# Optimization experiments

Measured on AMD Instinct MI355X. Metric: run time of the kernel, lower is better.

The kernel has to match this reference:

```python
import jax, jax.numpy as jnp
import numpy as np

N_VAR, N_CHK, DV, DC = 8192, 4096, 3, 6
N_EDGE = N_VAR * DV  # == N_CHK * DC = 24576
BATCH = 512
N_ITER = 5
EPS = 1e-12
ATANH_CLIP = 1.0 - 1e-7


def setup_inputs() -> dict:
    # Deterministic (3,6)-regular Tanner graph: each variable has DV edges,
    # each check has DC edges; edge-to-check assignment is a fixed permutation.
    rng = np.random.default_rng(0)
    var_index = np.repeat(np.arange(N_VAR, dtype=np.int32), DV)
    chk_index = rng.permutation(np.repeat(np.arange(N_CHK, dtype=np.int32), DC))
    key = jax.random.key(0)
    llr = jax.random.normal(key, (BATCH, N_VAR), dtype=jnp.float32) * 2.0
    return {
        "llr": llr,
        "var_index": jnp.asarray(var_index, jnp.int32),
        "chk_index": jnp.asarray(chk_index, jnp.int32),
    }


def reference(llr, var_index, chk_index):
    # Messages stored edge-major: [E, batch] so segment ops act on leading axis.
    x = llr.T                              # [N, batch]
    scattered = x[var_index]               # spa.scatter(llr) -> [E, batch]
    ext = jnp.zeros_like(scattered)        # extrinsic_value init
    outs = []
    for _ in range(N_ITER):
        # variable node process: leave-one-out sum of check->var extrinsics
        vsum = jax.ops.segment_sum(ext, var_index, num_segments=N_VAR)
        a_priori = vsum[var_index] - ext   # [E, batch]
        msg = a_priori + scattered
        # check node process: 2*atanh( prod_{e' in check, e'!=e} tanh(msg/2) )
        t = jnp.tanh(msg * 0.5)
        log_abs = jnp.log(jnp.abs(t) + EPS)
        sgn = jnp.sign(t)
        csum_log = jax.ops.segment_sum(log_abs, chk_index, num_segments=N_CHK)
        cprod_sgn = jax.ops.segment_prod(sgn, chk_index, num_segments=N_CHK)
        loo = jnp.exp(csum_log[chk_index] - log_abs) * (cprod_sgn[chk_index] * sgn)
        loo = jnp.clip(loo, -ATANH_CLIP, ATANH_CLIP)
        ext = 2.0 * jnp.arctanh(loo)
        # gather(extrinsic) + llr
        out = jax.ops.segment_sum(ext, var_index, num_segments=N_VAR) + x
        outs.append(out.T)                 # back to [batch, N]
    return jnp.stack(outs)                 # [N_ITER, batch, N]
```

## Files before the change

kernel.cpp:

```cpp
#include <hip/hip_runtime.h>
#include <math.h>

#define N_VAR 8192
#define N_CHK 4096
#define DC 6
#define DV 3
#define N_EDGE 24576
#define BATCH 512
#define N_ITER 5
#define CLIP_F 0.99999988f
#define NTHREADS 1024
#define VPT (N_VAR / NTHREADS)
#define CPT (N_CHK / NTHREADS)


__global__ void k_zero(int* __restrict__ cnt) {
    int i = blockIdx.x * blockDim.x + threadIdx.x;
    if (i < N_CHK) cnt[i] = 0;
}

__global__ void k_build(const int* __restrict__ chk_index,
                        int* __restrict__ cnt,
                        int* __restrict__ chk_edges) {
    int e = blockIdx.x * blockDim.x + threadIdx.x;
    if (e < N_EDGE) {
        int c = chk_index[e];
        int p = atomicAdd(&cnt[c], 1);
        chk_edges[c * DC + p] = e;
    }
}

__launch_bounds__(1024)
__global__ void k_spa(const float* __restrict__ llr,
                      const int* __restrict__ chk_edges,
                      float* __restrict__ out) {
    __shared__ float m[N_EDGE];
    const int b = blockIdx.x;
    const int tid = threadIdx.x;
    const float* __restrict__ lrow = llr + (size_t)b * N_VAR;
    float* __restrict__ orow = out + (size_t)b * N_VAR;

    float l[VPT], el[VPT];
    #pragma unroll
    for (int k = 0; k < VPT; ++k) {
        int v = tid + k * NTHREADS;
        l[k]  = lrow[v];
        el[k] = __expf(l[k]);
    }
    int ce[CPT][DC];
    #pragma unroll
    for (int k = 0; k < CPT; ++k) {
        int c = tid + k * NTHREADS;
        #pragma unroll
        for (int j = 0; j < DC; ++j) ce[k][j] = chk_edges[c * DC + j];
    }

    #pragma unroll 1
    for (int iter = 0; iter < N_ITER; ++iter) {
        #pragma unroll
        for (int k = 0; k < VPT; ++k) {
            int v = tid + k * NTHREADS;
            float E0, E1, E2;
            if (iter == 0) {
                E0 = E1 = E2 = el[k];
            } else {
                float q0 = m[3 * v], q1 = m[3 * v + 1], q2 = m[3 * v + 2];
                float q01 = q0 * q1, q12 = q1 * q2, q02 = q0 * q2;
                orow[(size_t)(iter - 1) * (BATCH * N_VAR) + v] = l[k] + __logf(q01 * q2);
                E0 = el[k] * q12; E1 = el[k] * q02; E2 = el[k] * q01;
            }
            m[3 * v]     = (E0 - 1.0f) * __builtin_amdgcn_rcpf(E0 + 1.0f);
            m[3 * v + 1] = (E1 - 1.0f) * __builtin_amdgcn_rcpf(E1 + 1.0f);
            m[3 * v + 2] = (E2 - 1.0f) * __builtin_amdgcn_rcpf(E2 + 1.0f);
        }
        __syncthreads();

        #pragma unroll
        for (int k = 0; k < CPT; ++k) {
            float t[DC];
            #pragma unroll
            for (int j = 0; j < DC; ++j) t[j] = m[ce[k][j]];
            float pre[DC + 1], suf[DC + 1];
            pre[0] = 1.0f; suf[DC] = 1.0f;
            #pragma unroll
            for (int j = 0; j < DC; ++j)      pre[j + 1] = pre[j] * t[j];
            #pragma unroll
            for (int j = DC - 1; j >= 0; --j) suf[j] = suf[j + 1] * t[j];
            bool zz = (pre[DC] == 0.0f);
            #pragma unroll
            for (int j = 0; j < DC; ++j) {
                float lo = pre[j] * suf[j + 1];
                lo = fminf(fmaxf(lo, -CLIP_F), CLIP_F);
                float q = (1.0f + lo) * __builtin_amdgcn_rcpf(1.0f - lo);
                m[ce[k][j]] = zz ? 1.0f : q;
            }
        }
        __syncthreads();
    }

    #pragma unroll
    for (int k = 0; k < VPT; ++k) {
        int v = tid + k * NTHREADS;
        float q3 = m[3 * v] * m[3 * v + 1] * m[3 * v + 2];
        orow[(size_t)(N_ITER - 1) * (BATCH * N_VAR) + v] = l[k] + __logf(q3);
    }
}

extern "C" void kernel_launch(void* const* d_in, const int* in_sizes, int n_in,
                              void* d_out, int out_size, void* d_ws, size_t ws_size,
                              hipStream_t stream) {
    const float* llr       = (const float*)d_in[0];
    const int*   chk_index = (const int*)d_in[2];
    float*       out       = (float*)d_out;

    int* cnt       = (int*)d_ws;
    int* chk_edges = cnt + N_CHK;

    k_zero <<<(N_CHK  + 255) / 256, 256, 0, stream>>>(cnt);
    k_build<<<(N_EDGE + 255) / 256, 256, 0, stream>>>(chk_index, cnt, chk_edges);
    k_spa  <<<BATCH, 1024, 0, stream>>>(llr, chk_edges, out);
}
```

Measured before the change: 145.2 us.

## Store SPA messages as fp16 square-root exponentials in a planar LDS layout

Messages in LDS are now stored as fp16 values of sqrt(exp(LLR)), clamped to the fp16 range, which halves LDS from 96KB to 48KB so two 1024-thread blocks can share a CU. The edge layout becomes planar (j*N_VAR+v), the tanh conversion moves into the check pass, and output is computed as 2*log of the product. Check-edge indices are reloaded from global memory every iteration instead of being held in registers, which lowers register pressure. fp16 with clamping adds precision loss and may change results near saturation, and the zero-product special case is removed.

Result: no change. 145.8 us (+0.4%).

```diff
diff --git a/kernel.cpp b/kernel.cpp
--- a/kernel.cpp
+++ b/kernel.cpp
@@ -1,10 +1,10 @@
 #include <hip/hip_runtime.h>
+#include <hip/hip_fp16.h>
 #include <math.h>
 
 #define N_VAR 8192
 #define N_CHK 4096
 #define DC 6
-#define DV 3
 #define N_EDGE 24576
 #define BATCH 512
 #define N_ITER 5
@@ -12,6 +12,9 @@
 #define NTHREADS 1024
 #define VPT (N_VAR / NTHREADS)
 #define CPT (N_CHK / NTHREADS)
+
+#define S_MIN 6.2e-5f
+#define S_MAX 6.0e4f
 
 
 __global__ void k_zero(int* __restrict__ cnt) {
@@ -26,83 +29,83 @@
     if (e < N_EDGE) {
         int c = chk_index[e];
         int p = atomicAdd(&cnt[c], 1);
-        chk_edges[c * DC + p] = e;
+        int v = e / 3, j = e - 3 * v;
+        chk_edges[c * DC + p] = j * N_VAR + v;
     }
 }
 
-__launch_bounds__(1024)
+__launch_bounds__(1024, 8)
 __global__ void k_spa(const float* __restrict__ llr,
                       const int* __restrict__ chk_edges,
                       float* __restrict__ out) {
-    __shared__ float m[N_EDGE];
+    __shared__ __half m[N_EDGE];
     const int b = blockIdx.x;
     const int tid = threadIdx.x;
     const float* __restrict__ lrow = llr + (size_t)b * N_VAR;
     float* __restrict__ orow = out + (size_t)b * N_VAR;
 
-    float l[VPT], el[VPT];
+    float sel[VPT];
+    #pragma unroll
+    for (int k = 0; k < VPT; ++k)
+        sel[k] = __expf(0.5f * lrow[tid + k * NTHREADS]);
+
     #pragma unroll
     for (int k = 0; k < VPT; ++k) {
         int v = tid + k * NTHREADS;
-        l[k]  = lrow[v];
-        el[k] = __expf(l[k]);
+        __half h = __float2half(sel[k]);
+        m[v] = h; m[N_VAR + v] = h; m[2 * N_VAR + v] = h;
     }
-    int ce[CPT][DC];
-    #pragma unroll
-    for (int k = 0; k < CPT; ++k) {
-        int c = tid + k * NTHREADS;
-        #pragma unroll
-        for (int j = 0; j < DC; ++j) ce[k][j] = chk_edges[c * DC + j];
-    }
+    __syncthreads();
 
     #pragma unroll 1
     for (int iter = 0; iter < N_ITER; ++iter) {
-        #pragma unroll
-        for (int k = 0; k < VPT; ++k) {
-            int v = tid + k * NTHREADS;
-            float E0, E1, E2;
-            if (iter == 0) {
-                E0 = E1 = E2 = el[k];
-            } else {
-                float q0 = m[3 * v], q1 = m[3 * v + 1], q2 = m[3 * v + 2];
-                float q01 = q0 * q1, q12 = q1 * q2, q02 = q0 * q2;
-                orow[(size_t)(iter - 1) * (BATCH * N_VAR) + v] = l[k] + __logf(q01 * q2);
-                E0 = el[k] * q12; E1 = el[k] * q02; E2 = el[k] * q01;
-            }
-            m[3 * v]     = (E0 - 1.0f) * __builtin_amdgcn_rcpf(E0 + 1.0f);
-            m[3 * v + 1] = (E1 - 1.0f) * __builtin_amdgcn_rcpf(E1 + 1.0f);
-            m[3 * v + 2] = (E2 - 1.0f) * __builtin_amdgcn_rcpf(E2 + 1.0f);
-        }
-        __syncthreads();
-
-        #pragma unroll
+        #pragma unroll 1
         for (int k = 0; k < CPT; ++k) {
+            int c = tid + k * NTHREADS;
+            const int* __restrict__ ep = chk_edges + c * DC;
+            int   idx[DC];
             float t[DC];
             #pragma unroll
-            for (int j = 0; j < DC; ++j) t[j] = m[ce[k][j]];
+            for (int j = 0; j < DC; ++j) idx[j] = ep[j];
+            #pragma unroll
+            for (int j = 0; j < DC; ++j) {
+                float s = __half2float(m[idx[j]]);
+                float E = s * s;
+                t[j] = (E - 1.0f) * __builtin_amdgcn_rcpf(E + 1.0f);
+            }
             float pre[DC + 1], suf[DC + 1];
             pre[0] = 1.0f; suf[DC] = 1.0f;
             #pragma unroll
             for (int j = 0; j < DC; ++j)      pre[j + 1] = pre[j] * t[j];
             #pragma unroll
             for (int j = DC - 1; j >= 0; --j) suf[j] = suf[j + 1] * t[j];
-            bool zz = (pre[DC] == 0.0f);
             #pragma unroll
             for (int j = 0; j < DC; ++j) {
                 float lo = pre[j] * suf[j + 1];
                 lo = fminf(fmaxf(lo, -CLIP_F), CLIP_F);
                 float q = (1.0f + lo) * __builtin_amdgcn_rcpf(1.0f - lo);
-                m[ce[k][j]] = zz ? 1.0f : q;
+                m[idx[j]] = __float2half(__builtin_amdgcn_sqrtf(q));
             }
         }
         __syncthreads();
-    }
 
-    #pragma unroll
-    for (int k = 0; k < VPT; ++k) {
-        int v = tid + k * NTHREADS;
-        float q3 = m[3 * v] * m[3 * v + 1] * m[3 * v + 2];
-        orow[(size_t)(N_ITER - 1) * (BATCH * N_VAR) + v] = l[k] + __logf(q3);
+        const bool last = (iter == N_ITER - 1);
+        #pragma unroll 1
+        for (int k = 0; k < VPT; ++k) {
+            int v = tid + k * NTHREADS;
+            float s0 = __half2float(m[v]);
+            float s1 = __half2float(m[N_VAR + v]);
+            float s2 = __half2float(m[2 * N_VAR + v]);
+            float s01 = s0 * s1, s12 = s1 * s2, s02 = s0 * s2;
+            orow[(size_t)iter * (BATCH * N_VAR) + v] = 2.0f * __logf(sel[k] * s01 * s2);
+            if (!last) {
+                float e0 = sel[k] * s12, e1 = sel[k] * s02, e2 = sel[k] * s01;
+                m[v]             = __float2half(fminf(fmaxf(e0, S_MIN), S_MAX));
+                m[N_VAR + v]     = __float2half(fminf(fmaxf(e1, S_MIN), S_MAX));
+                m[2 * N_VAR + v] = __float2half(fminf(fmaxf(e2, S_MIN), S_MAX));
+            }
+        }
+        if (!last) __syncthreads();
     }
 }
 
```
